# Kernel tuning notes

Measured on AMD Instinct MI355X. Metric: run time of the kernel, lower is better.

Reference implementation:

```python
import jax, jax.numpy as jnp
import numpy as np

B_SCALE = 1.3195079565048218
N_LEVELS = 16
BASE_RES = 16
MAX_PARAMS = 2 ** 19
N_POINTS = 1048576
PRIMES = (1, 2654435761, 805459861)  # uint32 hash primes (Instant-NGP)


def _level_meta():
    offsets, sizes, inds = [], [], []
    off = 0
    for i in range(N_LEVELS):
        res = int(np.ceil(BASE_RES * np.exp(i * np.log(B_SCALE)) - 1.0)) + 1
        p = res ** 3
        if p % 8 != 0:
            p = ((p + 7) // 8) * 8
        p = min(MAX_PARAMS, p)
        offsets.append(off)
        sizes.append(p)
        inds.append(res ** 3 <= p)  # dense (under_hash) vs hashed level
        off += p
    return offsets, sizes, inds, off


OFFSETS, SIZES, INDICATORS, TOTAL_PARAMS = _level_meta()
TOTAL_HASH_SIZE = TOTAL_PARAMS * 2  # == 11445040


def _encode_level(x01, table2, level):
    # x01: [N,3] in [0,1]; table2: [total_params, 2]
    scale = np.float32(BASE_RES * np.exp(level * np.log(B_SCALE)) - 1.0)
    resolution = np.uint32(np.ceil(scale) + 1)
    map_size = np.uint32(SIZES[level])
    pos = x01 * scale + 0.5
    grid_f = jnp.floor(pos)
    frac = pos - grid_f                           # [N,3] trilinear weights
    grid = grid_f.astype(jnp.uint32)              # [N,3]
    feat = jnp.zeros((x01.shape[0], 2), dtype=table2.dtype)
    primes = np.array(PRIMES, dtype=np.uint32)
    stride = np.array([1, int(resolution), int(resolution) * int(resolution)], dtype=np.uint32)
    for idx in range(8):  # 8 grid corners
        sel = np.array([(idx >> d) & 1 for d in range(3)], dtype=np.uint32)
        corner = grid + sel                       # [N,3] uint32
        w = jnp.prod(jnp.where(sel[None, :] == 1, frac, 1.0 - frac), axis=-1)  # [N]
        if INDICATORS[level]:
            c = corner * stride[None, :]
            h = c[:, 0] + c[:, 1] + c[:, 2]       # under_hash (dense indexing)
        else:
            c = corner * primes[None, :]          # uint32 wraparound multiply
            h = c[:, 0] ^ c[:, 1] ^ c[:, 2]       # fast_hash
        index = (h % map_size).astype(jnp.int32) + np.int32(OFFSETS[level])
        feat = feat + w[:, None] * table2[index]  # gather + trilinear blend
    return feat


def setup_inputs() -> dict:
    key = jax.random.key(0)
    k1, k2 = jax.random.split(key)
    positions = jax.random.uniform(k1, (N_POINTS, 3), dtype=jnp.float32, minval=-1.0, maxval=1.0)
    # random_initialize: (rand*2-1)*1e-4
    hash_table = jax.random.uniform(k2, (TOTAL_HASH_SIZE,), dtype=jnp.float32, minval=-1e-4, maxval=1e-4)
    return {"positions": positions, "hash_table": hash_table}


def reference(positions, hash_table):
    x01 = (positions + 1.0) * 0.5  # bound = 1
    table2 = hash_table.reshape(-1, 2)
    feats = [_encode_level(x01, table2, l) for l in range(N_LEVELS)]
    return jnp.concatenate(feats, axis=-1)  # [N, 32]
```

## Files before the change

### kernel.cpp

```cpp
#include <hip/hip_runtime.h>
#include <math.h>
#include <stdint.h>

#define NLV 16
#define NDENSE 6
#define NHASH 10
#define SORT_RES 32
#define NBINS (SORT_RES * SORT_RES * SORT_RES)

typedef float evf2 __attribute__((ext_vector_type(2)));
typedef unsigned int evu4 __attribute__((ext_vector_type(4)));
typedef _Float16 evh2 __attribute__((ext_vector_type(2)));

struct Params {
  float scale[NLV];
  uint32_t res[NLV];
  uint32_t msize[NLV];
  uint32_t offset[NLV];
};

struct ParamsD {
  float scale[NDENSE];
  uint32_t res[NDENSE];
  uint32_t msize[NDENSE];
  uint32_t offset[NDENSE];
};

__device__ __forceinline__ float ntload(const float* p) {
  return __builtin_nontemporal_load(p);
}

__device__ __forceinline__ uint32_t cell_key(float xr, float yr, float zr) {
  float x01 = (xr + 1.0f) * 0.5f;
  float y01 = (yr + 1.0f) * 0.5f;
  float z01 = (zr + 1.0f) * 0.5f;
  int cx = (int)(x01 * (float)SORT_RES);
  int cy = (int)(y01 * (float)SORT_RES);
  int cz = (int)(z01 * (float)SORT_RES);
  cx = cx < 0 ? 0 : (cx > SORT_RES-1 ? SORT_RES-1 : cx);
  cy = cy < 0 ? 0 : (cy > SORT_RES-1 ? SORT_RES-1 : cy);
  cz = cz < 0 ? 0 : (cz > SORT_RES-1 ? SORT_RES-1 : cz);
  return (uint32_t)(cx | (cy << 5) | (cz << 10));
}

__global__ __launch_bounds__(256) void zero_bins_kernel(uint32_t* bins) {
  int i = blockIdx.x * 256 + threadIdx.x;
  if (i < NBINS) bins[i] = 0u;
}

__global__ __launch_bounds__(256) void hist_kernel(
    const float* __restrict__ positions, uint32_t* __restrict__ bins, int n) {
  int t = blockIdx.x * 256 + threadIdx.x;
  int p0 = t * 4;
  if (p0 >= n) return;
  const float4 A = *reinterpret_cast<const float4*>(positions + 3*p0);
  const float4 B = *reinterpret_cast<const float4*>(positions + 3*p0 + 4);
  const float4 C = *reinterpret_cast<const float4*>(positions + 3*p0 + 8);
  atomicAdd(&bins[cell_key(A.x, A.y, A.z)], 1u);
  atomicAdd(&bins[cell_key(A.w, B.x, B.y)], 1u);
  atomicAdd(&bins[cell_key(B.z, B.w, C.x)], 1u);
  atomicAdd(&bins[cell_key(C.y, C.z, C.w)], 1u);
}

__global__ __launch_bounds__(1024) void scan_kernel(
    const uint32_t* __restrict__ bins, uint32_t* __restrict__ cursor) {
  __shared__ uint32_t lds[1024];
  int t = threadIdx.x;
  uint32_t local[32];
  uint32_t s = 0;
  #pragma unroll
  for (int j = 0; j < 32; ++j) { local[j] = bins[t*32 + j]; s += local[j]; }
  lds[t] = s;
  __syncthreads();
  for (int off = 1; off < 1024; off <<= 1) {
    uint32_t v = (t >= off) ? lds[t - off] : 0u;
    __syncthreads();
    lds[t] += v;
    __syncthreads();
  }
  uint32_t run = lds[t] - s;
  #pragma unroll
  for (int j = 0; j < 32; ++j) { cursor[t*32 + j] = run; run += local[j]; }
}

__global__ __launch_bounds__(256) void scatter_kernel(
    const float* __restrict__ positions, uint32_t* __restrict__ cursor,
    uint32_t* __restrict__ sidx, int n) {
  int t = blockIdx.x * 256 + threadIdx.x;
  int p0 = t * 4;
  if (p0 >= n) return;
  const float4 A = *reinterpret_cast<const float4*>(positions + 3*p0);
  const float4 B = *reinterpret_cast<const float4*>(positions + 3*p0 + 4);
  const float4 C = *reinterpret_cast<const float4*>(positions + 3*p0 + 8);
  float xs[4] = {A.x, A.w, B.z, C.y};
  float ys[4] = {A.y, B.x, B.w, C.z};
  float zs[4] = {A.z, B.y, C.x, C.w};
  #pragma unroll
  for (int q = 0; q < 4; ++q) {
    uint32_t k = cell_key(xs[q], ys[q], zs[q]);
    uint32_t dst = atomicAdd(&cursor[k], 1u);
    sidx[dst] = (uint32_t)(p0 + q);
  }
}

__global__ __launch_bounds__(256) void materialize_kernel(
    const float* __restrict__ positions, const uint32_t* __restrict__ sidx,
    evu4* __restrict__ spi, int n) {
  int p = blockIdx.x * 256 + threadIdx.x;
  if (p >= n) return;
  uint32_t si = sidx[p];
  evu4 v;
  v.x = __float_as_uint(positions[3*si]);
  v.y = __float_as_uint(positions[3*si + 1]);
  v.z = __float_as_uint(positions[3*si + 2]);
  v.w = si;
  spi[p] = v;
}

__global__ __launch_bounds__(256) void hash_level_kernel(
    const evu4* __restrict__ spi,
    const float* __restrict__ tbl,
    evh2* __restrict__ tmpH,
    float scale, uint32_t mask, int n)
{
  int t = blockIdx.x * 256 + threadIdx.x;
  int p0 = t * 2;
  if (p0 >= n) return;

  evu4 a = __builtin_nontemporal_load(spi + p0);
  evu4 b = (p0 + 1 < n) ? __builtin_nontemporal_load(spi + p0 + 1) : a;
  float xx[2] = {__uint_as_float(a.x), __uint_as_float(b.x)};
  float yy[2] = {__uint_as_float(a.y), __uint_as_float(b.y)};
  float zz[2] = {__uint_as_float(a.z), __uint_as_float(b.z)};

  float r0[2], r1[2];
  #pragma unroll
  for (int q = 0; q < 2; ++q) {
    float x = (xx[q] + 1.0f) * 0.5f;
    float y = (yy[q] + 1.0f) * 0.5f;
    float z = (zz[q] + 1.0f) * 0.5f;

    float px = x * scale + 0.5f;
    float py = y * scale + 0.5f;
    float pz = z * scale + 0.5f;
    float fx = floorf(px), fy = floorf(py), fz = floorf(pz);
    float tx = px - fx, ty = py - fy, tz = pz - fz;
    uint32_t gx = (uint32_t)fx, gy = (uint32_t)fy, gz = (uint32_t)fz;

    float wxa = 1.0f - tx, wxb = tx;
    float wy_[2] = {1.0f - ty, ty};
    float wz_[2] = {1.0f - tz, tz};

    float f0 = 0.0f, f1 = 0.0f;

    if ((gx & 1u) == 0u) {
      #pragma unroll
      for (int cyz = 0; cyz < 4; ++cyz) {
        uint32_t cy = gy + (cyz & 1u);
        uint32_t cz = gz + (cyz >> 1);
        uint32_t hy = (cy * 2654435761u) ^ (cz * 805459861u);
        uint32_t ha = (gx ^ hy) & mask;
        float wyz = wy_[cyz & 1u] * wz_[cyz >> 1];
        float wa = wxa * wyz, wb = wxb * wyz;
        const float4 t4 = *reinterpret_cast<const float4*>(tbl + 2u * (ha & ~1u));
        float2 ta, tb;
        if (ha & 1u) { ta.x = t4.z; ta.y = t4.w; tb.x = t4.x; tb.y = t4.y; }
        else         { ta.x = t4.x; ta.y = t4.y; tb.x = t4.z; tb.y = t4.w; }
        f0 += wa * ta.x; f1 += wa * ta.y;
        f0 += wb * tb.x; f1 += wb * tb.y;
      }
    } else {
      #pragma unroll
      for (int cyz = 0; cyz < 4; ++cyz) {
        uint32_t cy = gy + (cyz & 1u);
        uint32_t cz = gz + (cyz >> 1);
        uint32_t hy = (cy * 2654435761u) ^ (cz * 805459861u);
        uint32_t ha = (gx ^ hy) & mask;
        uint32_t hb = ((gx + 1u) ^ hy) & mask;
        float wyz = wy_[cyz & 1u] * wz_[cyz >> 1];
        float wa = wxa * wyz, wb = wxb * wyz;
        const float2 ta = *reinterpret_cast<const float2*>(tbl + 2u * ha);
        const float2 tb = *reinterpret_cast<const float2*>(tbl + 2u * hb);
        f0 += wa * ta.x; f1 += wa * ta.y;
        f0 += wb * tb.x; f1 += wb * tb.y;
      }
    }
    r0[q] = f0; r1[q] = f1;
  }

  evh2 v0; v0.x = (_Float16)r0[0]; v0.y = (_Float16)r1[0];
  __builtin_nontemporal_store(v0, tmpH + p0);
  if (p0 + 1 < n) {
    evh2 v1; v1.x = (_Float16)r0[1]; v1.y = (_Float16)r1[1];
    __builtin_nontemporal_store(v1, tmpH + p0 + 1);
  }
}

#define PBS 128
__global__ __launch_bounds__(PBS) void dense_pack2_kernel(
    const evu4* __restrict__ spi,
    const float* __restrict__ table,
    const evh2* __restrict__ tmpH,
    float* __restrict__ out,
    ParamsD prm, int n)
{
  __shared__ float lds[PBS * 33];
  __shared__ uint32_t lds_oi[PBS];
  int t = threadIdx.x;
  int base = blockIdx.x * PBS;
  int p = base + t;

  if (p < n) {
    evu4 a = __builtin_nontemporal_load(spi + p);
    float x = (__uint_as_float(a.x) + 1.0f) * 0.5f;
    float y = (__uint_as_float(a.y) + 1.0f) * 0.5f;
    float z = (__uint_as_float(a.z) + 1.0f) * 0.5f;
    lds_oi[t] = a.w;

    #pragma unroll
    for (int l = 0; l < NDENSE; ++l) {
      const float s = prm.scale[l];
      const uint32_t res = prm.res[l];
      const uint32_t ms = prm.msize[l];
      const float* __restrict__ tbl = table + 2u * prm.offset[l];
      const uint32_t res2 = res * res;

      float px = x * s + 0.5f;
      float py = y * s + 0.5f;
      float pz = z * s + 0.5f;
      float fx = floorf(px), fy = floorf(py), fz = floorf(pz);
      float tx = px - fx, ty = py - fy, tz = pz - fz;
      uint32_t gx = (uint32_t)fx, gy = (uint32_t)fy, gz = (uint32_t)fz;

      float wxa = 1.0f - tx, wxb = tx;
      float wy_[2] = {1.0f - ty, ty};
      float wz_[2] = {1.0f - tz, tz};

      float f0 = 0.0f, f1 = 0.0f;
      #pragma unroll
      for (int cyz = 0; cyz < 4; ++cyz) {
        uint32_t cy = gy + (cyz & 1u);
        uint32_t cz = gz + ((cyz >> 1) & 1u);
        uint32_t h = gx + cy * res + cz * res2;
        if (h >= ms) h -= ms;
        float wyz = wy_[cyz & 1u] * wz_[(cyz >> 1) & 1u];
        float2 ta, tb;
        if (h + 1u < ms) {
          const float4 t4 = *reinterpret_cast<const float4*>(tbl + 2u * h);
          ta.x = t4.x; ta.y = t4.y; tb.x = t4.z; tb.y = t4.w;
        } else {
          ta = *reinterpret_cast<const float2*>(tbl + 2u * h);
          tb = *reinterpret_cast<const float2*>(tbl);
        }
        float wa = wxa * wyz, wb = wxb * wyz;
        f0 += wa * ta.x; f1 += wa * ta.y;
        f0 += wb * tb.x; f1 += wb * tb.y;
      }
      lds[t*33 + 2*l]     = f0;
      lds[t*33 + 2*l + 1] = f1;
    }

    #pragma unroll
    for (int j = 0; j < NHASH; ++j) {
      evh2 v = __builtin_nontemporal_load(tmpH + (size_t)j * n + p);
      lds[t*33 + 12 + 2*j]     = (float)v.x;
      lds[t*33 + 12 + 2*j + 1] = (float)v.y;
    }
  }
  __syncthreads();

  if (base + PBS <= n) {
    int qr = t >> 3, r = t & 7;
    #pragma unroll
    for (int k = 0; k < 8; ++k) {
      int q = k * (PBS/8) + qr;
      uint32_t oi = lds_oi[q];
      float4 v = make_float4(lds[q*33 + r*4], lds[q*33 + r*4 + 1],
                             lds[q*33 + r*4 + 2], lds[q*33 + r*4 + 3]);
      reinterpret_cast<float4*>(out + (size_t)oi * 32u)[r] = v;
    }
  } else if (p < n) {
    uint32_t oi = lds_oi[t];
    float4* o = reinterpret_cast<float4*>(out + (size_t)oi * 32u);
    #pragma unroll
    for (int k = 0; k < 8; ++k)
      o[k] = make_float4(lds[t*33 + 4*k], lds[t*33 + 4*k + 1],
                         lds[t*33 + 4*k + 2], lds[t*33 + 4*k + 3]);
  }
}

__global__ __launch_bounds__(256) void hash_level_unsorted_kernel(
    const float* __restrict__ positions,
    const float* __restrict__ tbl,
    float2* __restrict__ tmp,
    float scale, uint32_t mask, int n)
{
  int t = blockIdx.x * 256 + threadIdx.x;
  int p0 = t * 2;
  if (p0 >= n) return;

  float xx[2], yy[2], zz[2];
  {
    evf2 a = __builtin_nontemporal_load(reinterpret_cast<const evf2*>(positions + 3*p0));
    evf2 b = __builtin_nontemporal_load(reinterpret_cast<const evf2*>(positions + 3*p0 + 2));
    evf2 c = __builtin_nontemporal_load(reinterpret_cast<const evf2*>(positions + 3*p0 + 4));
    xx[0] = a.x; yy[0] = a.y; zz[0] = b.x;
    xx[1] = b.y; yy[1] = c.x; zz[1] = c.y;
  }

  float r0[2], r1[2];
  #pragma unroll
  for (int q = 0; q < 2; ++q) {
    float x = (xx[q] + 1.0f) * 0.5f;
    float y = (yy[q] + 1.0f) * 0.5f;
    float z = (zz[q] + 1.0f) * 0.5f;
    float px = x * scale + 0.5f;
    float py = y * scale + 0.5f;
    float pz = z * scale + 0.5f;
    float fx = floorf(px), fy = floorf(py), fz = floorf(pz);
    float tx = px - fx, ty = py - fy, tz = pz - fz;
    uint32_t gx = (uint32_t)fx, gy = (uint32_t)fy, gz = (uint32_t)fz;
    float wxa = 1.0f - tx, wxb = tx;
    float wy_[2] = {1.0f - ty, ty};
    float wz_[2] = {1.0f - tz, tz};
    float f0 = 0.0f, f1 = 0.0f;
    #pragma unroll
    for (int cyz = 0; cyz < 4; ++cyz) {
      uint32_t cy = gy + (cyz & 1u);
      uint32_t cz = gz + (cyz >> 1);
      uint32_t hy = (cy * 2654435761u) ^ (cz * 805459861u);
      uint32_t ha = (gx ^ hy) & mask;
      uint32_t hb = ((gx + 1u) ^ hy) & mask;
      float wyz = wy_[cyz & 1u] * wz_[cyz >> 1];
      float wa = wxa * wyz, wb = wxb * wyz;
      const float2 ta = *reinterpret_cast<const float2*>(tbl + 2u * ha);
      const float2 tb = *reinterpret_cast<const float2*>(tbl + 2u * hb);
      f0 += wa * ta.x; f1 += wa * ta.y;
      f0 += wb * tb.x; f1 += wb * tb.y;
    }
    r0[q] = f0; r1[q] = f1;
  }
  evf2 v0; v0.x = r0[0]; v0.y = r1[0];
  __builtin_nontemporal_store(v0, reinterpret_cast<evf2*>(tmp + p0));
  if (p0 + 1 < n) {
    evf2 v1; v1.x = r0[1]; v1.y = r1[1];
    __builtin_nontemporal_store(v1, reinterpret_cast<evf2*>(tmp + p0 + 1));
  }
}

__global__ __launch_bounds__(256) void dense_unsorted_kernel(
    const float* __restrict__ positions,
    const float* __restrict__ table,
    float2* __restrict__ tmp,
    ParamsD prm, int n)
{
  int p = blockIdx.x * 256 + threadIdx.x;
  if (p >= n) return;

  float x = (ntload(positions + 3*p+0) + 1.0f) * 0.5f;
  float y = (ntload(positions + 3*p+1) + 1.0f) * 0.5f;
  float z = (ntload(positions + 3*p+2) + 1.0f) * 0.5f;

  #pragma unroll
  for (int l = 0; l < NDENSE; ++l) {
    const float s = prm.scale[l];
    const uint32_t res = prm.res[l];
    const uint32_t ms = prm.msize[l];
    const float* __restrict__ tbl = table + 2u * prm.offset[l];
    const uint32_t res2 = res * res;
    float px = x * s + 0.5f;
    float py = y * s + 0.5f;
    float pz = z * s + 0.5f;
    float fx = floorf(px), fy = floorf(py), fz = floorf(pz);
    float tx = px - fx, ty = py - fy, tz = pz - fz;
    uint32_t gx = (uint32_t)fx, gy = (uint32_t)fy, gz = (uint32_t)fz;
    float wxa = 1.0f - tx, wxb = tx;
    float wy_[2] = {1.0f - ty, ty};
    float wz_[2] = {1.0f - tz, tz};
    float f0 = 0.0f, f1 = 0.0f;
    #pragma unroll
    for (int cyz = 0; cyz < 4; ++cyz) {
      uint32_t cy = gy + (cyz & 1u);
      uint32_t cz = gz + ((cyz >> 1) & 1u);
      uint32_t h = gx + cy * res + cz * res2;
      if (h >= ms) h -= ms;
      float wyz = wy_[cyz & 1u] * wz_[(cyz >> 1) & 1u];
      float2 ta, tb;
      if (h + 1u < ms) {
        const float4 t4 = *reinterpret_cast<const float4*>(tbl + 2u * h);
        ta.x = t4.x; ta.y = t4.y; tb.x = t4.z; tb.y = t4.w;
      } else {
        ta = *reinterpret_cast<const float2*>(tbl + 2u * h);
        tb = *reinterpret_cast<const float2*>(tbl);
      }
      float wa = wxa * wyz, wb = wxb * wyz;
      f0 += wa * ta.x; f1 += wa * ta.y;
      f0 += wb * tb.x; f1 += wb * tb.y;
    }
    evf2 v; v.x = f0; v.y = f1;
    __builtin_nontemporal_store(v,
        reinterpret_cast<evf2*>(tmp + (size_t)(NHASH + l) * n + p));
  }
}

__global__ __launch_bounds__(256) void stream_pack_kernel(
    const float2* __restrict__ tmp, float* __restrict__ out, int n)
{
  int p = blockIdx.x * 256 + threadIdx.x;
  if (p >= n) return;
  evf2 dv[NDENSE];
  #pragma unroll
  for (int j = 0; j < NDENSE; ++j)
    dv[j] = __builtin_nontemporal_load(
        reinterpret_cast<const evf2*>(tmp + (size_t)(NHASH + j) * n + p));
  evf2 hv[NHASH];
  #pragma unroll
  for (int j = 0; j < NHASH; ++j)
    hv[j] = __builtin_nontemporal_load(
        reinterpret_cast<const evf2*>(tmp + (size_t)j * n + p));
  float4* o = reinterpret_cast<float4*>(out + (size_t)p * 32u);
  #pragma unroll
  for (int j = 0; j < 3; ++j)
    o[j] = make_float4(dv[2*j].x, dv[2*j].y, dv[2*j+1].x, dv[2*j+1].y);
  #pragma unroll
  for (int j = 0; j < 5; ++j)
    o[3 + j] = make_float4(hv[2*j].x, hv[2*j].y, hv[2*j+1].x, hv[2*j+1].y);
}

__global__ __launch_bounds__(256) void hash_enc_kernel(
    const float* __restrict__ positions,
    const float* __restrict__ table,
    float* __restrict__ out,
    Params prm, int n)
{
  int p = blockIdx.x * 256 + threadIdx.x;
  if (p >= n) return;

  float x = (positions[3*p+0] + 1.0f) * 0.5f;
  float y = (positions[3*p+1] + 1.0f) * 0.5f;
  float z = (positions[3*p+2] + 1.0f) * 0.5f;

  float acc[32];

  #pragma unroll
  for (int l = 0; l < NLV; ++l) {
    const float s = prm.scale[l];
    const uint32_t res = prm.res[l];
    const uint32_t ms = prm.msize[l];
    const uint32_t off = prm.offset[l];
    float px = x * s + 0.5f;
    float py = y * s + 0.5f;
    float pz = z * s + 0.5f;
    float fx = floorf(px), fy = floorf(py), fz = floorf(pz);
    float tx = px - fx, ty = py - fy, tz = pz - fz;
    uint32_t gx = (uint32_t)fx, gy = (uint32_t)fy, gz = (uint32_t)fz;
    float wx[2] = {1.0f - tx, tx};
    float wy[2] = {1.0f - ty, ty};
    float wz[2] = {1.0f - tz, tz};
    float f0 = 0.0f, f1 = 0.0f;
    #pragma unroll
    for (int c = 0; c < 8; ++c) {
      uint32_t cx = gx + (c & 1u);
      uint32_t cy = gy + ((c >> 1) & 1u);
      uint32_t cz = gz + ((c >> 2) & 1u);
      uint32_t h;
      if (l < NDENSE) {
        h = cx + cy * res + cz * res * res;
        if (h >= ms) h -= ms;
      } else {
        h = cx ^ (cy * 2654435761u) ^ (cz * 805459861u);
        h &= (ms - 1u);
      }
      float w = (wx[c & 1u] * wy[(c >> 1) & 1u]) * wz[(c >> 2) & 1u];
      const float2 t = *reinterpret_cast<const float2*>(table + 2u * (h + off));
      f0 += w * t.x;
      f1 += w * t.y;
    }
    acc[2*l]   = f0;
    acc[2*l+1] = f1;
  }

  float4* o = reinterpret_cast<float4*>(out + (size_t)p * 32u);
  #pragma unroll
  for (int k = 0; k < 8; ++k)
    o[k] = make_float4(acc[4*k+0], acc[4*k+1], acc[4*k+2], acc[4*k+3]);
}

extern "C" void kernel_launch(void* const* d_in, const int* in_sizes, int n_in,
                              void* d_out, int out_size, void* d_ws, size_t ws_size,
                              hipStream_t stream) {
  const float* positions = (const float*)d_in[0];
  const float* table     = (const float*)d_in[1];
  float* out             = (float*)d_out;
  int n = in_sizes[0] / 3;

  Params prm;
  const double lnb = log(1.3195079565048218);
  uint32_t off = 0;
  for (int l = 0; l < NLV; ++l) {
    double sd = 16.0 * exp((double)l * lnb) - 1.0;
    uint32_t res_meta = (uint32_t)ceil(sd) + 1u;
    uint64_t p3 = (uint64_t)res_meta * res_meta * res_meta;
    uint64_t ps = (p3 % 8ull) ? ((p3 + 7ull) / 8ull) * 8ull : p3;
    if (ps > (1ull << 19)) ps = 1ull << 19;
    float sf = (float)sd;
    uint32_t res_enc = (uint32_t)(ceilf(sf) + 1.0f);
    prm.scale[l]  = sf;
    prm.res[l]    = res_enc;
    prm.msize[l]  = (uint32_t)ps;
    prm.offset[l] = off;
    off += (uint32_t)ps;
  }
  ParamsD pd;
  for (int l = 0; l < NDENSE; ++l) {
    pd.scale[l] = prm.scale[l]; pd.res[l] = prm.res[l];
    pd.msize[l] = prm.msize[l]; pd.offset[l] = prm.offset[l];
  }

  dim3 block(256);
  dim3 gfull((n + 255) / 256);
  dim3 ghash((n/2 + 255) / 256);
  dim3 gquad((n/4 + 255) / 256);
  dim3 gpack((n + PBS - 1) / PBS);

  size_t tmp_b  = (size_t)NHASH * n * sizeof(evh2);
  size_t sp_off = tmp_b;
  size_t si_off = sp_off + (size_t)n * sizeof(evu4);
  size_t bn_off = si_off + (size_t)n * sizeof(uint32_t);
  size_t cu_off = bn_off + (size_t)NBINS * sizeof(uint32_t);
  size_t total  = cu_off + (size_t)NBINS * sizeof(uint32_t);
  size_t ws16   = (size_t)NLV * n * sizeof(float2);

  char* wsb = (char*)d_ws;

  if (ws_size >= total && (n % 4) == 0) {
    evh2*     tmpH   = (evh2*)wsb;
    evu4*     spi    = (evu4*)(wsb + sp_off);
    uint32_t* sidx   = (uint32_t*)(wsb + si_off);
    uint32_t* bins   = (uint32_t*)(wsb + bn_off);
    uint32_t* cursor = (uint32_t*)(wsb + cu_off);

    hipLaunchKernelGGL(zero_bins_kernel, dim3((NBINS + 255) / 256), block, 0, stream, bins);
    hipLaunchKernelGGL(hist_kernel, gquad, block, 0, stream, positions, bins, n);
    hipLaunchKernelGGL(scan_kernel, dim3(1), dim3(1024), 0, stream, bins, cursor);
    hipLaunchKernelGGL(scatter_kernel, gquad, block, 0, stream,
                       positions, cursor, sidx, n);
    hipLaunchKernelGGL(materialize_kernel, gfull, block, 0, stream,
                       positions, sidx, spi, n);

    for (int l = NDENSE; l < NLV; ++l) {
      hipLaunchKernelGGL(hash_level_kernel, ghash, block, 0, stream,
                         spi, table + 2u * prm.offset[l],
                         tmpH + (size_t)(l - NDENSE) * n,
                         prm.scale[l], prm.msize[l] - 1u, n);
    }
    hipLaunchKernelGGL(dense_pack2_kernel, gpack, dim3(PBS), 0, stream,
                       spi, table, tmpH, out, pd, n);
  } else if (ws_size >= ws16 && (n % 2) == 0) {
    float2* tmp = (float2*)d_ws;
    for (int l = NDENSE; l < NLV; ++l) {
      hipLaunchKernelGGL(hash_level_unsorted_kernel, ghash, block, 0, stream,
                         positions, table + 2u * prm.offset[l],
                         tmp + (size_t)(l - NDENSE) * n,
                         prm.scale[l], prm.msize[l] - 1u, n);
    }
    hipLaunchKernelGGL(dense_unsorted_kernel, gfull, block, 0, stream,
                       positions, table, tmp, pd, n);
    hipLaunchKernelGGL(stream_pack_kernel, gfull, block, 0, stream,
                       tmp, out, n);
  } else {
    hipLaunchKernelGGL(hash_enc_kernel, gfull, block, 0, stream,
                       positions, table, out, prm, n);
  }
}
```

Before: 444.9 us.

## Fuse scatter with materialize, merge hash levels, add XCD block swizzle

The scatter kernel now writes the sorted position-plus-index records directly, so the separate materialize pass and the sidx buffer are gone. The first six hashed levels, which all use a 2^19-entry mask, are computed in one multi-level kernel that reads each sorted point once. All hot kernels remap block IDs so that contiguous sorted ranges land on the same XCD for better L2 locality, and the unsorted fallback path is removed. The costs are more register pressure in the merged kernel and scattered 16-byte writes in scatter.

```diff
diff --git a/kernel.cpp b/kernel.cpp
--- a/kernel.cpp
+++ b/kernel.cpp
@@ -5,12 +5,14 @@
 #define NLV 16
 #define NDENSE 6
 #define NHASH 10
+#define NMERGE 6
 #define SORT_RES 32
 #define NBINS (SORT_RES * SORT_RES * SORT_RES)
 
 typedef float evf2 __attribute__((ext_vector_type(2)));
 typedef unsigned int evu4 __attribute__((ext_vector_type(4)));
 typedef _Float16 evh2 __attribute__((ext_vector_type(2)));
+typedef _Float16 evh4 __attribute__((ext_vector_type(4)));
 
 struct Params {
   float scale[NLV];
@@ -26,8 +28,19 @@
   uint32_t offset[NDENSE];
 };
 
+struct ParamsH {
+  float scale[NMERGE];
+  uint32_t offset[NMERGE];
+};
+
 __device__ __forceinline__ float ntload(const float* p) {
   return __builtin_nontemporal_load(p);
+}
+
+__device__ __forceinline__ int xcd_swz(int bid, int nwg) {
+  int q = nwg >> 3, r = nwg & 7;
+  int x = bid & 7, i = bid >> 3;
+  return (x < r ? x * (q + 1) : r * (q + 1) + (x - r) * q) + i;
 }
 
 __device__ __forceinline__ uint32_t cell_key(float xr, float yr, float zr) {
@@ -85,7 +98,7 @@
 
 __global__ __launch_bounds__(256) void scatter_kernel(
     const float* __restrict__ positions, uint32_t* __restrict__ cursor,
-    uint32_t* __restrict__ sidx, int n) {
+    evu4* __restrict__ spi, int n) {
   int t = blockIdx.x * 256 + threadIdx.x;
   int p0 = t * 4;
   if (p0 >= n) return;
@@ -99,22 +112,98 @@
   for (int q = 0; q < 4; ++q) {
     uint32_t k = cell_key(xs[q], ys[q], zs[q]);
     uint32_t dst = atomicAdd(&cursor[k], 1u);
-    sidx[dst] = (uint32_t)(p0 + q);
-  }
-}
-
-__global__ __launch_bounds__(256) void materialize_kernel(
-    const float* __restrict__ positions, const uint32_t* __restrict__ sidx,
-    evu4* __restrict__ spi, int n) {
-  int p = blockIdx.x * 256 + threadIdx.x;
-  if (p >= n) return;
-  uint32_t si = sidx[p];
-  evu4 v;
-  v.x = __float_as_uint(positions[3*si]);
-  v.y = __float_as_uint(positions[3*si + 1]);
-  v.z = __float_as_uint(positions[3*si + 2]);
-  v.w = si;
-  spi[p] = v;
+    evu4 v;
+    v.x = __float_as_uint(xs[q]);
+    v.y = __float_as_uint(ys[q]);
+    v.z = __float_as_uint(zs[q]);
+    v.w = (uint32_t)(p0 + q);
+    spi[dst] = v;
+  }
+}
+
+__device__ __forceinline__ void hash_feat(
+    float x01, float y01, float z01, float scale, uint32_t mask,
+    const float* __restrict__ tbl, float& f0, float& f1)
+{
+  float px = x01 * scale + 0.5f;
+  float py = y01 * scale + 0.5f;
+  float pz = z01 * scale + 0.5f;
+  float fx = floorf(px), fy = floorf(py), fz = floorf(pz);
+  float tx = px - fx, ty = py - fy, tz = pz - fz;
+  uint32_t gx = (uint32_t)fx, gy = (uint32_t)fy, gz = (uint32_t)fz;
+
+  float wxa = 1.0f - tx, wxb = tx;
+  float wy_[2] = {1.0f - ty, ty};
+  float wz_[2] = {1.0f - tz, tz};
+
+  f0 = 0.0f; f1 = 0.0f;
+  if ((gx & 1u) == 0u) {
+    #pragma unroll
+    for (int cyz = 0; cyz < 4; ++cyz) {
+      uint32_t cy = gy + (cyz & 1u);
+      uint32_t cz = gz + (cyz >> 1);
+      uint32_t hy = (cy * 2654435761u) ^ (cz * 805459861u);
+      uint32_t ha = (gx ^ hy) & mask;
+      float wyz = wy_[cyz & 1u] * wz_[cyz >> 1];
+      float wa = wxa * wyz, wb = wxb * wyz;
+      const float4 t4 = *reinterpret_cast<const float4*>(tbl + 2u * (ha & ~1u));
+      float2 ta, tb;
+      if (ha & 1u) { ta.x = t4.z; ta.y = t4.w; tb.x = t4.x; tb.y = t4.y; }
+      else         { ta.x = t4.x; ta.y = t4.y; tb.x = t4.z; tb.y = t4.w; }
+      f0 += wa * ta.x; f1 += wa * ta.y;
+      f0 += wb * tb.x; f1 += wb * tb.y;
+    }
+  } else {
+    #pragma unroll
+    for (int cyz = 0; cyz < 4; ++cyz) {
+      uint32_t cy = gy + (cyz & 1u);
+      uint32_t cz = gz + (cyz >> 1);
+      uint32_t hy = (cy * 2654435761u) ^ (cz * 805459861u);
+      uint32_t ha = (gx ^ hy) & mask;
+      uint32_t hb = ((gx + 1u) ^ hy) & mask;
+      float wyz = wy_[cyz & 1u] * wz_[cyz >> 1];
+      float wa = wxa * wyz, wb = wxb * wyz;
+      const float2 ta = *reinterpret_cast<const float2*>(tbl + 2u * ha);
+      const float2 tb = *reinterpret_cast<const float2*>(tbl + 2u * hb);
+      f0 += wa * ta.x; f1 += wa * ta.y;
+      f0 += wb * tb.x; f1 += wb * tb.y;
+    }
+  }
+}
+
+__global__ __launch_bounds__(256) void hash_multi_kernel(
+    const evu4* __restrict__ spi,
+    const float* __restrict__ table,
+    evh2* __restrict__ tmpH,
+    ParamsH ph, uint32_t mask, int n)
+{
+  int bid = xcd_swz(blockIdx.x, gridDim.x);
+  int t = bid * 256 + threadIdx.x;
+  int p0 = t * 2;
+  if (p0 >= n) return;
+
+  evu4 a = __builtin_nontemporal_load(spi + p0);
+  evu4 b = __builtin_nontemporal_load(spi + p0 + 1);
+  float x0 = (__uint_as_float(a.x) + 1.0f) * 0.5f;
+  float y0 = (__uint_as_float(a.y) + 1.0f) * 0.5f;
+  float z0 = (__uint_as_float(a.z) + 1.0f) * 0.5f;
+  float x1 = (__uint_as_float(b.x) + 1.0f) * 0.5f;
+  float y1 = (__uint_as_float(b.y) + 1.0f) * 0.5f;
+  float z1 = (__uint_as_float(b.z) + 1.0f) * 0.5f;
+
+  #pragma unroll
+  for (int l = 0; l < NMERGE; ++l) {
+    const float s = ph.scale[l];
+    const float* __restrict__ tbl = table + 2u * ph.offset[l];
+    float f00, f01, f10, f11;
+    hash_feat(x0, y0, z0, s, mask, tbl, f00, f01);
+    hash_feat(x1, y1, z1, s, mask, tbl, f10, f11);
+    evh4 v;
+    v.x = (_Float16)f00; v.y = (_Float16)f01;
+    v.z = (_Float16)f10; v.w = (_Float16)f11;
+    __builtin_nontemporal_store(v,
+        reinterpret_cast<evh4*>(tmpH + (size_t)l * n + p0));
+  }
 }
 
 __global__ __launch_bounds__(256) void hash_level_kernel(
@@ -123,77 +212,24 @@
     evh2* __restrict__ tmpH,
     float scale, uint32_t mask, int n)
 {
-  int t = blockIdx.x * 256 + threadIdx.x;
+  int bid = xcd_swz(blockIdx.x, gridDim.x);
+  int t = bid * 256 + threadIdx.x;
   int p0 = t * 2;
   if (p0 >= n) return;
 
   evu4 a = __builtin_nontemporal_load(spi + p0);
-  evu4 b = (p0 + 1 < n) ? __builtin_nontemporal_load(spi + p0 + 1) : a;
-  float xx[2] = {__uint_as_float(a.x), __uint_as_float(b.x)};
-  float yy[2] = {__uint_as_float(a.y), __uint_as_float(b.y)};
-  float zz[2] = {__uint_as_float(a.z), __uint_as_float(b.z)};
-
-  float r0[2], r1[2];
-  #pragma unroll
-  for (int q = 0; q < 2; ++q) {
-    float x = (xx[q] + 1.0f) * 0.5f;
-    float y = (yy[q] + 1.0f) * 0.5f;
-    float z = (zz[q] + 1.0f) * 0.5f;
-
-    float px = x * scale + 0.5f;
-    float py = y * scale + 0.5f;
-    float pz = z * scale + 0.5f;
-    float fx = floorf(px), fy = floorf(py), fz = floorf(pz);
-    float tx = px - fx, ty = py - fy, tz = pz - fz;
-    uint32_t gx = (uint32_t)fx, gy = (uint32_t)fy, gz = (uint32_t)fz;
-
-    float wxa = 1.0f - tx, wxb = tx;
-    float wy_[2] = {1.0f - ty, ty};
-    float wz_[2] = {1.0f - tz, tz};
-
-    float f0 = 0.0f, f1 = 0.0f;
-
-    if ((gx & 1u) == 0u) {
-      #pragma unroll
-      for (int cyz = 0; cyz < 4; ++cyz) {
-        uint32_t cy = gy + (cyz & 1u);
-        uint32_t cz = gz + (cyz >> 1);
-        uint32_t hy = (cy * 2654435761u) ^ (cz * 805459861u);
-        uint32_t ha = (gx ^ hy) & mask;
-        float wyz = wy_[cyz & 1u] * wz_[cyz >> 1];
-        float wa = wxa * wyz, wb = wxb * wyz;
-        const float4 t4 = *reinterpret_cast<const float4*>(tbl + 2u * (ha & ~1u));
-        float2 ta, tb;
-        if (ha & 1u) { ta.x = t4.z; ta.y = t4.w; tb.x = t4.x; tb.y = t4.y; }
-        else         { ta.x = t4.x; ta.y = t4.y; tb.x = t4.z; tb.y = t4.w; }
-        f0 += wa * ta.x; f1 += wa * ta.y;
-        f0 += wb * tb.x; f1 += wb * tb.y;
-      }
-    } else {
-      #pragma unroll
-      for (int cyz = 0; cyz < 4; ++cyz) {
-        uint32_t cy = gy + (cyz & 1u);
-        uint32_t cz = gz + (cyz >> 1);
-        uint32_t hy = (cy * 2654435761u) ^ (cz * 805459861u);
-        uint32_t ha = (gx ^ hy) & mask;
-        uint32_t hb = ((gx + 1u) ^ hy) & mask;
-        float wyz = wy_[cyz & 1u] * wz_[cyz >> 1];
-        float wa = wxa * wyz, wb = wxb * wyz;
-        const float2 ta = *reinterpret_cast<const float2*>(tbl + 2u * ha);
-        const float2 tb = *reinterpret_cast<const float2*>(tbl + 2u * hb);
-        f0 += wa * ta.x; f1 += wa * ta.y;
-        f0 += wb * tb.x; f1 += wb * tb.y;
-      }
-    }
-    r0[q] = f0; r1[q] = f1;
-  }
-
-  evh2 v0; v0.x = (_Float16)r0[0]; v0.y = (_Float16)r1[0];
-  __builtin_nontemporal_store(v0, tmpH + p0);
-  if (p0 + 1 < n) {
-    evh2 v1; v1.x = (_Float16)r0[1]; v1.y = (_Float16)r1[1];
-    __builtin_nontemporal_store(v1, tmpH + p0 + 1);
-  }
+  evu4 b = __builtin_nontemporal_load(spi + p0 + 1);
+  float f00, f01, f10, f11;
+  hash_feat((__uint_as_float(a.x) + 1.0f) * 0.5f,
+            (__uint_as_float(a.y) + 1.0f) * 0.5f,
+            (__uint_as_float(a.z) + 1.0f) * 0.5f, scale, mask, tbl, f00, f01);
+  hash_feat((__uint_as_float(b.x) + 1.0f) * 0.5f,
+            (__uint_as_float(b.y) + 1.0f) * 0.5f,
+            (__uint_as_float(b.z) + 1.0f) * 0.5f, scale, mask, tbl, f10, f11);
+  evh4 v;
+  v.x = (_Float16)f00; v.y = (_Float16)f01;
+  v.z = (_Float16)f10; v.w = (_Float16)f11;
+  __builtin_nontemporal_store(v, reinterpret_cast<evh4*>(tmpH + p0));
 }
 
 #define PBS 128
@@ -207,7 +243,7 @@
   __shared__ float lds[PBS * 33];
   __shared__ uint32_t lds_oi[PBS];
   int t = threadIdx.x;
-  int base = blockIdx.x * PBS;
+  int base = xcd_swz(blockIdx.x, gridDim.x) * PBS;
   int p = base + t;
 
   if (p < n) {
@@ -289,144 +325,6 @@
   }
 }
 
-__global__ __launch_bounds__(256) void hash_level_unsorted_kernel(
-    const float* __restrict__ positions,
-    const float* __restrict__ tbl,
-    float2* __restrict__ tmp,
-    float scale, uint32_t mask, int n)
-{
-  int t = blockIdx.x * 256 + threadIdx.x;
-  int p0 = t * 2;
-  if (p0 >= n) return;
-
-  float xx[2], yy[2], zz[2];
-  {
-    evf2 a = __builtin_nontemporal_load(reinterpret_cast<const evf2*>(positions + 3*p0));
-    evf2 b = __builtin_nontemporal_load(reinterpret_cast<const evf2*>(positions + 3*p0 + 2));
-    evf2 c = __builtin_nontemporal_load(reinterpret_cast<const evf2*>(positions + 3*p0 + 4));
-    xx[0] = a.x; yy[0] = a.y; zz[0] = b.x;
-    xx[1] = b.y; yy[1] = c.x; zz[1] = c.y;
-  }
-
-  float r0[2], r1[2];
-  #pragma unroll
-  for (int q = 0; q < 2; ++q) {
-    float x = (xx[q] + 1.0f) * 0.5f;
-    float y = (yy[q] + 1.0f) * 0.5f;
-    float z = (zz[q] + 1.0f) * 0.5f;
-    float px = x * scale + 0.5f;
-    float py = y * scale + 0.5f;
-    float pz = z * scale + 0.5f;
-    float fx = floorf(px), fy = floorf(py), fz = floorf(pz);
-    float tx = px - fx, ty = py - fy, tz = pz - fz;
-    uint32_t gx = (uint32_t)fx, gy = (uint32_t)fy, gz = (uint32_t)fz;
-    float wxa = 1.0f - tx, wxb = tx;
-    float wy_[2] = {1.0f - ty, ty};
-    float wz_[2] = {1.0f - tz, tz};
-    float f0 = 0.0f, f1 = 0.0f;
-    #pragma unroll
-    for (int cyz = 0; cyz < 4; ++cyz) {
-      uint32_t cy = gy + (cyz & 1u);
-      uint32_t cz = gz + (cyz >> 1);
-      uint32_t hy = (cy * 2654435761u) ^ (cz * 805459861u);
-      uint32_t ha = (gx ^ hy) & mask;
-      uint32_t hb = ((gx + 1u) ^ hy) & mask;
-      float wyz = wy_[cyz & 1u] * wz_[cyz >> 1];
-      float wa = wxa * wyz, wb = wxb * wyz;
-      const float2 ta = *reinterpret_cast<const float2*>(tbl + 2u * ha);
-      const float2 tb = *reinterpret_cast<const float2*>(tbl + 2u * hb);
-      f0 += wa * ta.x; f1 += wa * ta.y;
-      f0 += wb * tb.x; f1 += wb * tb.y;
-    }
-    r0[q] = f0; r1[q] = f1;
-  }
-  evf2 v0; v0.x = r0[0]; v0.y = r1[0];
-  __builtin_nontemporal_store(v0, reinterpret_cast<evf2*>(tmp + p0));
-  if (p0 + 1 < n) {
-    evf2 v1; v1.x = r0[1]; v1.y = r1[1];
-    __builtin_nontemporal_store(v1, reinterpret_cast<evf2*>(tmp + p0 + 1));
-  }
-}
-
-__global__ __launch_bounds__(256) void dense_unsorted_kernel(
-    const float* __restrict__ positions,
-    const float* __restrict__ table,
-    float2* __restrict__ tmp,
-    ParamsD prm, int n)
-{
-  int p = blockIdx.x * 256 + threadIdx.x;
-  if (p >= n) return;
-
-  float x = (ntload(positions + 3*p+0) + 1.0f) * 0.5f;
-  float y = (ntload(positions + 3*p+1) + 1.0f) * 0.5f;
-  float z = (ntload(positions + 3*p+2) + 1.0f) * 0.5f;
-
-  #pragma unroll
-  for (int l = 0; l < NDENSE; ++l) {
-    const float s = prm.scale[l];
-    const uint32_t res = prm.res[l];
-    const uint32_t ms = prm.msize[l];
-    const float* __restrict__ tbl = table + 2u * prm.offset[l];
-    const uint32_t res2 = res * res;
-    float px = x * s + 0.5f;
-    float py = y * s + 0.5f;
-    float pz = z * s + 0.5f;
-    float fx = floorf(px), fy = floorf(py), fz = floorf(pz);
-    float tx = px - fx, ty = py - fy, tz = pz - fz;
-    uint32_t gx = (uint32_t)fx, gy = (uint32_t)fy, gz = (uint32_t)fz;
-    float wxa = 1.0f - tx, wxb = tx;
-    float wy_[2] = {1.0f - ty, ty};
-    float wz_[2] = {1.0f - tz, tz};
-    float f0 = 0.0f, f1 = 0.0f;
-    #pragma unroll
-    for (int cyz = 0; cyz < 4; ++cyz) {
-      uint32_t cy = gy + (cyz & 1u);
-      uint32_t cz = gz + ((cyz >> 1) & 1u);
-      uint32_t h = gx + cy * res + cz * res2;
-      if (h >= ms) h -= ms;
-      float wyz = wy_[cyz & 1u] * wz_[(cyz >> 1) & 1u];
-      float2 ta, tb;
-      if (h + 1u < ms) {
-        const float4 t4 = *reinterpret_cast<const float4*>(tbl + 2u * h);
-        ta.x = t4.x; ta.y = t4.y; tb.x = t4.z; tb.y = t4.w;
-      } else {
-        ta = *reinterpret_cast<const float2*>(tbl + 2u * h);
-        tb = *reinterpret_cast<const float2*>(tbl);
-      }
-      float wa = wxa * wyz, wb = wxb * wyz;
-      f0 += wa * ta.x; f1 += wa * ta.y;
-      f0 += wb * tb.x; f1 += wb * tb.y;
-    }
-    evf2 v; v.x = f0; v.y = f1;
-    __builtin_nontemporal_store(v,
-        reinterpret_cast<evf2*>(tmp + (size_t)(NHASH + l) * n + p));
-  }
-}
-
-__global__ __launch_bounds__(256) void stream_pack_kernel(
-    const float2* __restrict__ tmp, float* __restrict__ out, int n)
-{
-  int p = blockIdx.x * 256 + threadIdx.x;
-  if (p >= n) return;
-  evf2 dv[NDENSE];
-  #pragma unroll
-  for (int j = 0; j < NDENSE; ++j)
-    dv[j] = __builtin_nontemporal_load(
-        reinterpret_cast<const evf2*>(tmp + (size_t)(NHASH + j) * n + p));
-  evf2 hv[NHASH];
-  #pragma unroll
-  for (int j = 0; j < NHASH; ++j)
-    hv[j] = __builtin_nontemporal_load(
-        reinterpret_cast<const evf2*>(tmp + (size_t)j * n + p));
-  float4* o = reinterpret_cast<float4*>(out + (size_t)p * 32u);
-  #pragma unroll
-  for (int j = 0; j < 3; ++j)
-    o[j] = make_float4(dv[2*j].x, dv[2*j].y, dv[2*j+1].x, dv[2*j+1].y);
-  #pragma unroll
-  for (int j = 0; j < 5; ++j)
-    o[3 + j] = make_float4(hv[2*j].x, hv[2*j].y, hv[2*j+1].x, hv[2*j+1].y);
-}
-
 __global__ __launch_bounds__(256) void hash_enc_kernel(
     const float* __restrict__ positions,
     const float* __restrict__ table,
@@ -516,6 +414,11 @@
     pd.scale[l] = prm.scale[l]; pd.res[l] = prm.res[l];
     pd.msize[l] = prm.msize[l]; pd.offset[l] = prm.offset[l];
   }
+  ParamsH ph;
+  for (int l = 0; l < NMERGE; ++l) {
+    ph.scale[l]  = prm.scale[NDENSE + l];
+    ph.offset[l] = prm.offset[NDENSE + l];
+  }
 
   dim3 block(256);
   dim3 gfull((n + 255) / 256);
@@ -525,18 +428,15 @@
 
   size_t tmp_b  = (size_t)NHASH * n * sizeof(evh2);
   size_t sp_off = tmp_b;
-  size_t si_off = sp_off + (size_t)n * sizeof(evu4);
-  size_t bn_off = si_off + (size_t)n * sizeof(uint32_t);
+  size_t bn_off = sp_off + (size_t)n * sizeof(evu4);
   size_t cu_off = bn_off + (size_t)NBINS * sizeof(uint32_t);
   size_t total  = cu_off + (size_t)NBINS * sizeof(uint32_t);
-  size_t ws16   = (size_t)NLV * n * sizeof(float2);
 
   char* wsb = (char*)d_ws;
 
   if (ws_size >= total && (n % 4) == 0) {
     evh2*     tmpH   = (evh2*)wsb;
     evu4*     spi    = (evu4*)(wsb + sp_off);
-    uint32_t* sidx   = (uint32_t*)(wsb + si_off);
     uint32_t* bins   = (uint32_t*)(wsb + bn_off);
     uint32_t* cursor = (uint32_t*)(wsb + cu_off);
 
@@ -544,11 +444,11 @@
     hipLaunchKernelGGL(hist_kernel, gquad, block, 0, stream, positions, bins, n);
     hipLaunchKernelGGL(scan_kernel, dim3(1), dim3(1024), 0, stream, bins, cursor);
     hipLaunchKernelGGL(scatter_kernel, gquad, block, 0, stream,
-                       positions, cursor, sidx, n);
-    hipLaunchKernelGGL(materialize_kernel, gfull, block, 0, stream,
-                       positions, sidx, spi, n);
-
-    for (int l = NDENSE; l < NLV; ++l) {
+                       positions, cursor, spi, n);
+
+    hipLaunchKernelGGL(hash_multi_kernel, ghash, block, 0, stream,
+                       spi, table, tmpH, ph, prm.msize[NDENSE] - 1u, n);
+    for (int l = NDENSE + NMERGE; l < NLV; ++l) {
       hipLaunchKernelGGL(hash_level_kernel, ghash, block, 0, stream,
                          spi, table + 2u * prm.offset[l],
                          tmpH + (size_t)(l - NDENSE) * n,
@@ -556,18 +456,6 @@
     }
     hipLaunchKernelGGL(dense_pack2_kernel, gpack, dim3(PBS), 0, stream,
                        spi, table, tmpH, out, pd, n);
-  } else if (ws_size >= ws16 && (n % 2) == 0) {
-    float2* tmp = (float2*)d_ws;
-    for (int l = NDENSE; l < NLV; ++l) {
-      hipLaunchKernelGGL(hash_level_unsorted_kernel, ghash, block, 0, stream,
-                         positions, table + 2u * prm.offset[l],
-                         tmp + (size_t)(l - NDENSE) * n,
-                         prm.scale[l], prm.msize[l] - 1u, n);
-    }
-    hipLaunchKernelGGL(dense_unsorted_kernel, gfull, block, 0, stream,
-                       positions, table, tmp, pd, n);
-    hipLaunchKernelGGL(stream_pack_kernel, gfull, block, 0, stream,
-                       tmp, out, n);
   } else {
     hipLaunchKernelGGL(hash_enc_kernel, gfull, block, 0, stream,
                        positions, table, out, prm, n);
```

Result: faster. 432.6 us (-2.8%).
